# Kernel tuning notes

Hardware: AMD Instinct MI355X
Metric: run time of the kernel (lower is better)

The kernel has to match this reference:

```python
import jax, jax.numpy as jnp
import numpy as np

B, IN, OUT, E, H, K = 8192, 1024, 256, 16, 512, 3
EPS = 1e-10


def setup_inputs() -> dict:
    key = jax.random.key(0)
    ks = jax.random.split(key, 5)
    scaled = lambda k, shape, fan: jax.random.normal(k, shape, jnp.float32) / np.sqrt(fan)
    return {
        "x": jax.random.normal(ks[0], (B, IN), jnp.float32),
        # torch init is zeros for w_gate (degenerate ties); use small random for a meaningful reference
        "w_gate": jax.random.normal(ks[1], (IN, E), jnp.float32) * 0.02,
        "W1": scaled(ks[2], (E, IN, H), IN),
        "b1": jnp.zeros((E, H), jnp.float32),
        "W2": scaled(ks[3], (E, H, OUT), H),
        "b2": jnp.zeros((E, OUT), jnp.float32),
    }


def _cv_squared(v):
    # torch .var() is unbiased (ddof=1)
    return jnp.var(v, ddof=1) / (jnp.mean(v) ** 2 + EPS)


def reference(x, w_gate, W1, b1, W2, b2):
    # --- top-k gating (eval mode: clean logits, no noise) ---
    logits = x @ w_gate                                   # [B, E]
    top_vals, top_idx = jax.lax.top_k(logits, K)          # [B, K]
    top_gates = jax.nn.softmax(top_vals, axis=-1)         # softmax over selected k
    rows = jnp.arange(logits.shape[0])[:, None]
    gates = jnp.zeros_like(logits).at[rows, top_idx].set(top_gates)  # sparse gates [B, E]

    # --- load-balancing loss ---
    importance = gates.sum(0)
    load = (gates > 0).sum(0).astype(jnp.float32)         # _gates_to_load (eval path)
    loss = _cv_squared(importance) + _cv_squared(load)

    # --- experts (MLP stand-in; dense compute, sparse combine via zero gates) ---
    h = jax.nn.relu(jnp.einsum('bi,eih->beh', x, W1) + b1)  # [B, E, H]
    expert_out = jnp.einsum('beh,eho->beo', h, W2) + b2     # [B, E, OUT]

    # combine: equivalent to SparseDispatcher gather/split/scatter-add with gate weighting
    y = jnp.einsum('be,beo->bo', gates, expert_out)         # [B, OUT]
    return y, loss
```

## Files before the change

kernel.cpp:

```cpp
#include <hip/hip_runtime.h>

#define B_ 8192
#define IN_ 1024
#define OUT_ 256
#define E_ 16
#define KTOP 3
#define H_ 512
#define MAXSLOTS 26624
#define NTILES 208
#define HBLK 32
#define GBLK 512

typedef __bf16 bf16;
typedef __bf16 bf16x4 __attribute__((ext_vector_type(4)));
typedef __bf16 bf16x8 __attribute__((ext_vector_type(8)));
typedef float f32x4 __attribute__((ext_vector_type(4)));

__device__ __forceinline__ void async16(const bf16* g, bf16* l) {
    __builtin_amdgcn_global_load_lds(
        (const __attribute__((address_space(1))) void*)g,
        (__attribute__((address_space(3))) void*)l,
        16, 0, 0);
}

__global__ __launch_bounds__(256) void k_stage1(
    const float* __restrict__ x, const float* __restrict__ wg,
    const float* __restrict__ W1, const float* __restrict__ W2,
    bf16* __restrict__ xbf, int* __restrict__ top_idx, float* __restrict__ top_gate,
    int* __restrict__ partial,
    bf16* __restrict__ w1t, bf16* __restrict__ w2t,
    int* __restrict__ row_ids, bf16* __restrict__ zero_row, int* __restrict__ tile_expert) {
    __shared__ __align__(16) float smem[16448];
    __shared__ int lcnt[16];
    int bx = blockIdx.x;
    int t = threadIdx.x;
    if (bx < GBLK) {
        float4* swgT4 = (float4*)smem;
        const float4* wg4 = (const float4*)wg;
        if (t < 16) lcnt[t] = 0;
#pragma unroll
        for (int i = 0; i < 16; i++) {
            int p = (t & 3) * 4 + ((t >> 2) & 3);
            int slot = i * 16 + (t >> 4);
            swgT4[p * 257 + slot] = wg4[i * 256 + t];
        }
        __syncthreads();
        int wv = t >> 6, lane = t & 63;
#pragma unroll
        for (int pr = 0; pr < 2; ++pr) {
            int row = bx * 16 + wv * 4 + pr * 2;
            const float4* xra = (const float4*)(x + (size_t)row * IN_);
            const float4* xrb = (const float4*)(x + (size_t)(row + 1) * IN_);
            float4 xa[4], xb4[4];
#pragma unroll
            for (int q = 0; q < 4; q++) { xa[q] = xra[lane + 64 * q]; xb4[q] = xrb[lane + 64 * q]; }
#pragma unroll
            for (int q = 0; q < 4; q++) {
                bf16x4 ca, cb;
                ca[0] = (bf16)xa[q].x; ca[1] = (bf16)xa[q].y; ca[2] = (bf16)xa[q].z; ca[3] = (bf16)xa[q].w;
                cb[0] = (bf16)xb4[q].x; cb[1] = (bf16)xb4[q].y; cb[2] = (bf16)xb4[q].z; cb[3] = (bf16)xb4[q].w;
                *(bf16x4*)(xbf + (size_t)row * IN_ + (size_t)(lane + 64 * q) * 4) = ca;
                *(bf16x4*)(xbf + (size_t)(row + 1) * IN_ + (size_t)(lane + 64 * q) * 4) = cb;
            }
            float acca[16], accb[16];
#pragma unroll
            for (int e = 0; e < 16; e++) { acca[e] = 0.f; accb[e] = 0.f; }
#pragma unroll
            for (int q = 0; q < 4; q++) {
                float sa[4] = {xa[q].x, xa[q].y, xa[q].z, xa[q].w};
                float sb[4] = {xb4[q].x, xb4[q].y, xb4[q].z, xb4[q].w};
#pragma unroll
                for (int jj = 0; jj < 4; jj++) {
#pragma unroll
                    for (int e4 = 0; e4 < 4; e4++) {
                        float4 w4 = swgT4[(e4 * 4 + jj) * 257 + lane + 64 * q];
                        acca[e4 * 4 + 0] += sa[jj] * w4.x;
                        acca[e4 * 4 + 1] += sa[jj] * w4.y;
                        acca[e4 * 4 + 2] += sa[jj] * w4.z;
                        acca[e4 * 4 + 3] += sa[jj] * w4.w;
                        accb[e4 * 4 + 0] += sb[jj] * w4.x;
                        accb[e4 * 4 + 1] += sb[jj] * w4.y;
                        accb[e4 * 4 + 2] += sb[jj] * w4.z;
                        accb[e4 * 4 + 3] += sb[jj] * w4.w;
                    }
                }
            }
#pragma unroll
            for (int e = 0; e < 16; e++) {
#pragma unroll
                for (int s = 32; s > 0; s >>= 1) {
                    acca[e] += __shfl_xor(acca[e], s, 64);
                    accb[e] += __shfl_xor(accb[e], s, 64);
                }
            }
            if (lane < 2) {
                float v[16];
#pragma unroll
                for (int e = 0; e < 16; e++) v[e] = lane ? accb[e] : acca[e];
                int rsel = row + lane;
                int idx[KTOP];
                float val[KTOP];
#pragma unroll
                for (int k = 0; k < KTOP; k++) {
                    int best = 0;
                    float bv = v[0];
                    for (int e = 1; e < 16; e++) {
                        if (v[e] > bv) { bv = v[e]; best = e; }
                    }
                    idx[k] = best; val[k] = bv; v[best] = -1e30f;
                }
                float e1 = __expf(val[1] - val[0]);
                float e2 = __expf(val[2] - val[0]);
                float inv = 1.f / (1.f + e1 + e2);
                float g[KTOP] = {inv, e1 * inv, e2 * inv};
#pragma unroll
                for (int k = 0; k < KTOP; k++) {
                    top_idx[rsel * KTOP + k] = idx[k];
                    top_gate[rsel * KTOP + k] = g[k];
                    atomicAdd(&lcnt[idx[k]], 1);
                }
            }
        }
        __syncthreads();
        if (t < 16) partial[bx * 16 + t] = lcnt[t];
        return;
    }
    if (bx >= 3072) {
        if (bx < 3176) {
            row_ids[(bx - 3072) * 256 + t] = -1;
        } else {
#pragma unroll
            for (int i = 0; i < 4; i++) zero_row[t * 4 + i] = (bf16)0.f;
            if (t < NTILES) tile_expert[t] = -1;
        }
        return;
    }
    float (*tile)[65] = (float(*)[65])smem;
    const float* in; bf16* out; int Kd, Nd, e, tk, tn;
    if (bx < 2560) {
        int b1x = bx - 512;
        in = W1; out = w1t; Kd = IN_; Nd = H_;
        e = b1x >> 7; int tt = b1x & 127; tk = tt >> 3; tn = tt & 7;
    } else {
        int b2x = bx - 2560;
        in = W2; out = w2t; Kd = H_; Nd = OUT_;
        e = b2x >> 5; int tt = b2x & 31; tk = tt >> 2; tn = tt & 3;
    }
    const float* src = in + ((size_t)e * Kd + tk * 64) * Nd + (size_t)tn * 64;
    {
        int c4 = (t & 15) * 4;
#pragma unroll
        for (int p = 0; p < 4; p++) {
            int kr = p * 16 + (t >> 4);
            float4 v = *(const float4*)(src + (size_t)kr * Nd + c4);
            tile[kr][c4 + 0] = v.x;
            tile[kr][c4 + 1] = v.y;
            tile[kr][c4 + 2] = v.z;
            tile[kr][c4 + 3] = v.w;
        }
    }
    __syncthreads();
    bf16* dst = out + ((size_t)e * Nd + tn * 64) * Kd + (size_t)tk * 64;
    {
        int k8 = (t & 7) * 8;
#pragma unroll
        for (int p = 0; p < 2; p++) {
            int n = p * 32 + (t >> 3);
            bf16x8 o;
#pragma unroll
            for (int j = 0; j < 8; j++) o[j] = (bf16)tile[k8 + j][n];
            *(bf16x8*)(dst + (size_t)n * Kd + k8) = o;
        }
    }
}

__global__ __launch_bounds__(256) void k_scatterscan(
    const int* __restrict__ top_idx, const float* __restrict__ top_gate,
    const int* __restrict__ partial,
    int* __restrict__ counts, int* __restrict__ tile_expert,
    int* __restrict__ row_ids, int* __restrict__ rowslot,
    float* __restrict__ partial_imp) {
    __shared__ int segsum[32][16];
    __shared__ int tote[16];
    __shared__ int sbase[16];
    __shared__ int lcnt[16];
    __shared__ float limp[16];
    int t = threadIdx.x;
    int blk = blockIdx.x;
    int e = t & 15, sg2 = t >> 4;
#pragma unroll
    for (int h = 0; h < 2; h++) {
        int seg = sg2 + h * 16;
        int s = 0;
#pragma unroll
        for (int i = 0; i < 16; i++) s += partial[(seg * 16 + i) * 16 + e];
        segsum[seg][e] = s;
    }
    if (t < 16) { lcnt[t] = 0; limp[t] = 0.f; }
    __syncthreads();
    if (t < 16) {
        int total = 0, pre = 0;
        for (int sg = 0; sg < 32; sg++) {
            int v = segsum[sg][t];
            total += v;
            if (sg < blk) pre += v;
        }
        tote[t] = total;
        segsum[0][t] = pre;
    }
    __syncthreads();
    if (t < 16) {
        int off = 0;
        for (int ee = 0; ee < 16; ee++) {
            if (ee == t) break;
            off += (tote[ee] + 127) & ~127;
        }
        sbase[t] = off + segsum[0][t];
        if (blk == 0) {
            counts[t] = tote[t];
            int pd = (tote[t] + 127) & ~127;
            for (int tt = off >> 7; tt < (off + pd) >> 7; ++tt) tile_expert[tt] = t;
        }
    }
    __syncthreads();
#pragma unroll
    for (int j = 0; j < 3; j++) {
        int gid = blk * 768 + j * 256 + t;
        int ee = top_idx[gid];
        float g = top_gate[gid];
        int rank = atomicAdd(&lcnt[ee], 1);
        atomicAdd(&limp[ee], g);
        int slot = sbase[ee] + rank;
        row_ids[slot] = gid / KTOP;
        rowslot[gid] = slot;
    }
    __syncthreads();
    if (t < 16) partial_imp[blk * 16 + t] = limp[t];
}

#define VWAIT(N) asm volatile("s_waitcnt vmcnt(" #N ")" ::: "memory")
__global__ __launch_bounds__(512) void k_fused(
    const bf16* __restrict__ xbf, const bf16* __restrict__ w1t,
    const float* __restrict__ b1, const bf16* __restrict__ w2t,
    const float* __restrict__ b2, const int* __restrict__ row_ids,
    const int* __restrict__ tile_expert, const bf16* __restrict__ zero_row,
    bf16* __restrict__ eout) {
    int bid = blockIdx.x;
    int tile = (bid & 7) * (NTILES / 8) + (bid >> 3);
    int e = tile_expert[tile];
    if (e < 0) return;
    int slot_base = tile * 128;
    __shared__ __align__(16) bf16 smem[69632];
    bf16* hs = smem;
    bf16* pb0 = smem + 32768;
    bf16* pb1 = smem + 32768 + 12288;
    bf16* pb2 = smem + 32768 + 24576;
    int t = threadIdx.x;
    int cg = (t & 3) ^ ((t >> 3) & 3);
    int rid = row_ids[slot_base + (t >> 2)];
    const bf16* gA = ((rid >= 0) ? xbf + (size_t)rid * IN_ : zero_row) + cg * 8;
    const bf16* gB1[2];
    const bf16* gB2[2];
#pragma unroll
    for (int j = 0; j < 2; j++) {
        int m = j * 128 + (t >> 2);
        gB1[j] = w1t + ((size_t)e * H_ + m) * IN_ + cg * 8;
        gB2[j] = w2t + ((size_t)e * OUT_ + m) * H_ + cg * 8;
    }
    int w = t >> 6, lane = t & 63;
    int wm = (w & 1) * 64, wn = (w >> 1) * 64;
    int lm = lane & 15, lq = lane >> 4;
    int aidx[4], bidx[4], hrow[4], hx[4];
#pragma unroll
    for (int i = 0; i < 4; i++) {
        int ra = wm + i * 16 + lm;
        int rb = wn + i * 16 + lm;
        aidx[i] = ra * 4 + (lq ^ ((ra >> 1) & 3));
        bidx[i] = rb * 4 + (lq ^ ((rb >> 1) & 3));
        hrow[i] = ra * 32;
        hx[i] = ra & 7;
    }
    float rbias1[2][4], rbias2[4];
#pragma unroll
    for (int c2 = 0; c2 < 2; ++c2)
#pragma unroll
        for (int ni = 0; ni < 4; ++ni) rbias1[c2][ni] = b1[e * H_ + c2 * 256 + wn + ni * 16 + lm];
#pragma unroll
    for (int ni = 0; ni < 4; ++ni) rbias2[ni] = b2[e * OUT_ + wn + ni * 16 + lm];
#pragma unroll
    for (int c2 = 0; c2 < 2; ++c2)
#pragma unroll
        for (int ni = 0; ni < 4; ++ni) asm volatile("" : "+v"(rbias1[c2][ni]));
#pragma unroll
    for (int ni = 0; ni < 4; ++ni) asm volatile("" : "+v"(rbias2[ni]));

    auto stageG1 = [&](bf16* buf, int c, int k) {
        async16(gA + k * 32, buf + t * 8);
        async16(gB1[0] + (size_t)c * (256 * IN_) + k * 32, buf + 4096 + t * 8);
        async16(gB1[1] + (size_t)c * (256 * IN_) + k * 32, buf + 4096 + (512 + t) * 8);
    };
    auto stageG2 = [&](bf16* buf, int c, int s) {
        const bf16* p0 = gB2[0] + c * 256 + s * 32;
        async16(p0, buf + t * 8);
        async16(gB2[1] + c * 256 + s * 32, buf + (512 + t) * 8);
        async16(p0, buf + t * 8);
    };

    f32x4 acc2[4][4] = {};
    bf16 *bufA = pb0, *bufB = pb1, *bufC = pb2;
    stageG1(bufA, 0, 0);
    stageG1(bufB, 0, 1);
#pragma unroll
    for (int c = 0; c < 2; ++c) {
        f32x4 acc1[4][4] = {};
        for (int k = 0; k < 32; ++k) {
            VWAIT(3);
            __builtin_amdgcn_s_barrier();
            __builtin_amdgcn_sched_barrier(0);
            const bf16x8* Av = (const bf16x8*)bufA;
            const bf16x8* Bv = (const bf16x8*)(bufA + 4096);
            bf16x8 af[4], bfv[4];
#pragma unroll
            for (int i = 0; i < 4; i++) af[i] = Av[aidx[i]];
#pragma unroll
            for (int i = 0; i < 4; i++) bfv[i] = Bv[bidx[i]];
            __builtin_amdgcn_s_setprio(1);
#pragma unroll
            for (int mi = 0; mi < 4; mi++)
#pragma unroll
                for (int ni = 0; ni < 4; ni++)
                    acc1[mi][ni] = __builtin_amdgcn_mfma_f32_16x16x32_bf16(af[mi], bfv[ni], acc1[mi][ni], 0, 0, 0);
            __builtin_amdgcn_s_setprio(0);
            if (k < 30) stageG1(bufC, c, k + 2);
            else        stageG2(bufC, c, k - 30);
            bf16* tmpb = bufA; bufA = bufB; bufB = bufC; bufC = tmpb;
        }
#pragma unroll
        for (int mi = 0; mi < 4; mi++) {
#pragma unroll
            for (int ni = 0; ni < 4; ni++) {
                int col = wn + ni * 16 + lm;
                float bias = rbias1[c][ni];
#pragma unroll
                for (int r = 0; r < 4; r++) {
                    int row = wm + mi * 16 + lq * 4 + r;
                    float v = acc1[mi][ni][r] + bias;
                    v = v > 0.f ? v : 0.f;
                    hs[row * 256 + (((col >> 3) ^ (row & 7)) << 3) + (col & 7)] = (bf16)v;
                }
            }
        }
        asm volatile("s_waitcnt lgkmcnt(0)" ::: "memory");
#pragma unroll
        for (int s = 0; s < 8; ++s) {
            if (c == 1 && s == 7) { VWAIT(0); } else { VWAIT(3); }
            __builtin_amdgcn_s_barrier();
            __builtin_amdgcn_sched_barrier(0);
            const bf16x8* Hv = (const bf16x8*)hs;
            const bf16x8* B2v = (const bf16x8*)bufA;
            bf16x8 af[4], bfv[4];
#pragma unroll
            for (int i = 0; i < 4; i++) af[i] = Hv[hrow[i] + ((s * 4 + lq) ^ hx[i])];
#pragma unroll
            for (int i = 0; i < 4; i++) bfv[i] = B2v[bidx[i]];
            __builtin_amdgcn_s_setprio(1);
#pragma unroll
            for (int mi = 0; mi < 4; mi++)
#pragma unroll
                for (int ni = 0; ni < 4; ni++)
                    acc2[mi][ni] = __builtin_amdgcn_mfma_f32_16x16x32_bf16(af[mi], bfv[ni], acc2[mi][ni], 0, 0, 0);
            __builtin_amdgcn_s_setprio(0);
            if (s < 6)       stageG2(bufC, c, s + 2);
            else if (c == 0) stageG1(bufC, 1, s - 6);
            bf16* tmpb = bufA; bufA = bufB; bufB = bufC; bufC = tmpb;
        }
    }
#pragma unroll
    for (int mi = 0; mi < 4; mi++) {
#pragma unroll
        for (int ni = 0; ni < 4; ni++) {
            int colg = wn + ni * 16 + lm;
            float bias = rbias2[ni];
#pragma unroll
            for (int r = 0; r < 4; r++) {
                int rowl = wm + mi * 16 + lq * 4 + r;
                eout[(size_t)(slot_base + rowl) * OUT_ + colg] = (bf16)(acc2[mi][ni][r] + bias);
            }
        }
    }
}

__global__ __launch_bounds__(256) void k_combine(
    const bf16* __restrict__ eout, const int* __restrict__ rowslot,
    const float* __restrict__ top_gate, float* __restrict__ y,
    const float* __restrict__ partial_imp, const int* __restrict__ counts,
    float* __restrict__ loss_out) {
    int t = threadIdx.x;
    if (blockIdx.x == B_ / 4) {
        __shared__ float imp[16];
        if (t < 16) {
            float s = 0.f;
#pragma unroll
            for (int b = 0; b < HBLK; b++) s += partial_imp[b * 16 + t];
            imp[t] = s;
        }
        __syncthreads();
        if (t == 0) {
            float si = 0.f, sl = 0.f;
            for (int e = 0; e < E_; e++) { si += imp[e]; sl += (float)counts[e]; }
            float mi_ = si / (float)E_, ml_ = sl / (float)E_;
            float vi = 0.f, vl = 0.f;
            for (int e = 0; e < E_; e++) {
                float d = imp[e] - mi_; vi += d * d;
                float d2 = (float)counts[e] - ml_; vl += d2 * d2;
            }
            vi /= (float)(E_ - 1); vl /= (float)(E_ - 1);
            *loss_out = vi / (mi_ * mi_ + 1e-10f) + vl / (ml_ * ml_ + 1e-10f);
        }
        return;
    }
    int b = blockIdx.x * 4 + (t >> 6);
    int lane = t & 63;
    int s0 = rowslot[b * 3], s1 = rowslot[b * 3 + 1], s2 = rowslot[b * 3 + 2];
    float g0 = top_gate[b * 3], g1 = top_gate[b * 3 + 1], g2 = top_gate[b * 3 + 2];
    bf16x4 v0 = *(const bf16x4*)(eout + (size_t)s0 * OUT_ + lane * 4);
    bf16x4 v1 = *(const bf16x4*)(eout + (size_t)s1 * OUT_ + lane * 4);
    bf16x4 v2 = *(const bf16x4*)(eout + (size_t)s2 * OUT_ + lane * 4);
    float4 r;
    r.x = g0 * (float)v0[0] + g1 * (float)v1[0] + g2 * (float)v2[0];
    r.y = g0 * (float)v0[1] + g1 * (float)v1[1] + g2 * (float)v2[1];
    r.z = g0 * (float)v0[2] + g1 * (float)v1[2] + g2 * (float)v2[2];
    r.w = g0 * (float)v0[3] + g1 * (float)v1[3] + g2 * (float)v2[3];
    ((float4*)y)[(size_t)b * 64 + lane] = r;
}

extern "C" void kernel_launch(void* const* d_in, const int* in_sizes, int n_in,
                              void* d_out, int out_size, void* d_ws, size_t ws_size,
                              hipStream_t stream) {
    (void)in_sizes; (void)n_in; (void)out_size; (void)ws_size;
    const float* x = (const float*)d_in[0];
    const float* wgate = (const float*)d_in[1];
    const float* W1 = (const float*)d_in[2];
    const float* b1 = (const float*)d_in[3];
    const float* W2 = (const float*)d_in[4];
    const float* b2 = (const float*)d_in[5];
    float* y = (float*)d_out;

    char* p = (char*)d_ws;
    auto alloc = [&](size_t bytes) {
        char* q = p;
        p += (bytes + 255) & ~(size_t)255;
        return q;
    };
    bf16* xbf = (bf16*)alloc((size_t)B_ * IN_ * 2);
    bf16* w1t = (bf16*)alloc((size_t)E_ * H_ * IN_ * 2);
    bf16* w2t = (bf16*)alloc((size_t)E_ * OUT_ * H_ * 2);
    bf16* eout = (bf16*)alloc((size_t)MAXSLOTS * OUT_ * 2);
    int* row_ids = (int*)alloc((size_t)MAXSLOTS * 4);
    int* rowslot = (int*)alloc((size_t)B_ * KTOP * 4);
    int* top_idx = (int*)alloc((size_t)B_ * KTOP * 4);
    float* top_gate = (float*)alloc((size_t)B_ * KTOP * 4);
    int* counts = (int*)alloc(E_ * 4);
    int* partial = (int*)alloc((size_t)GBLK * E_ * 4);
    float* partial_imp = (float*)alloc(HBLK * E_ * 4);
    int* tile_expert = (int*)alloc(NTILES * 4);
    bf16* zero_row = (bf16*)alloc(IN_ * 2);

    k_stage1<<<dim3(3177), dim3(256), 0, stream>>>(
        x, wgate, W1, W2, xbf, top_idx, top_gate, partial, w1t, w2t,
        row_ids, zero_row, tile_expert);
    k_scatterscan<<<dim3(HBLK), dim3(256), 0, stream>>>(
        top_idx, top_gate, partial, counts, tile_expert, row_ids, rowslot, partial_imp);
    k_fused<<<dim3(NTILES), dim3(512), 0, stream>>>(
        xbf, w1t, b1, w2t, b2, row_ids, tile_expert, zero_row, eout);
    k_combine<<<dim3(B_ / 4 + 1), dim3(256), 0, stream>>>(
        eout, rowslot, top_gate, y, partial_imp, counts, y + (size_t)B_ * OUT_);
}
```

Baseline: 183.3 us.

## Fuse gated combine into expert GEMM epilogue via atomic adds to output

The expert kernel now multiplies each output row by its gate and atomically accumulates it straight into y, instead of writing a bf16 eout buffer that a separate combine kernel re-reads. y is zeroed by extra blocks in the first stage kernel, and the combine kernel shrinks to a one-block loss kernel. This removes the eout round trip and one large launch, but adds float atomics (three writers per token) with non-deterministic summation order and scattered per-element atomic traffic. The s_setprio hints around the MFMA loops are also dropped.

```diff
diff --git a/kernel.cpp b/kernel.cpp
--- a/kernel.cpp
+++ b/kernel.cpp
@@ -29,7 +29,8 @@
     bf16* __restrict__ xbf, int* __restrict__ top_idx, float* __restrict__ top_gate,
     int* __restrict__ partial,
     bf16* __restrict__ w1t, bf16* __restrict__ w2t,
-    int* __restrict__ row_ids, bf16* __restrict__ zero_row, int* __restrict__ tile_expert) {
+    int* __restrict__ row_ids, bf16* __restrict__ zero_row, int* __restrict__ tile_expert,
+    float* __restrict__ y) {
     __shared__ __align__(16) float smem[16448];
     __shared__ int lcnt[16];
     int bx = blockIdx.x;
@@ -128,10 +129,15 @@
     if (bx >= 3072) {
         if (bx < 3176) {
             row_ids[(bx - 3072) * 256 + t] = -1;
-        } else {
+        } else if (bx == 3176) {
 #pragma unroll
             for (int i = 0; i < 4; i++) zero_row[t * 4 + i] = (bf16)0.f;
             if (t < NTILES) tile_expert[t] = -1;
+        } else {
+            float4* y4 = (float4*)y + (size_t)(bx - 3177) * 1024;
+            float4 z = {0.f, 0.f, 0.f, 0.f};
+#pragma unroll
+            for (int i = 0; i < 4; i++) y4[i * 256 + t] = z;
         }
         return;
     }
@@ -178,7 +184,7 @@
     const int* __restrict__ top_idx, const float* __restrict__ top_gate,
     const int* __restrict__ partial,
     int* __restrict__ counts, int* __restrict__ tile_expert,
-    int* __restrict__ row_ids, int* __restrict__ rowslot,
+    int* __restrict__ row_ids, float* __restrict__ slot_gate,
     float* __restrict__ partial_imp) {
     __shared__ int segsum[32][16];
     __shared__ int tote[16];
@@ -232,7 +238,7 @@
         atomicAdd(&limp[ee], g);
         int slot = sbase[ee] + rank;
         row_ids[slot] = gid / KTOP;
-        rowslot[gid] = slot;
+        slot_gate[slot] = g;
     }
     __syncthreads();
     if (t < 16) partial_imp[blk * 16 + t] = limp[t];
@@ -243,8 +249,9 @@
     const bf16* __restrict__ xbf, const bf16* __restrict__ w1t,
     const float* __restrict__ b1, const bf16* __restrict__ w2t,
     const float* __restrict__ b2, const int* __restrict__ row_ids,
+    const float* __restrict__ slot_gate,
     const int* __restrict__ tile_expert, const bf16* __restrict__ zero_row,
-    bf16* __restrict__ eout) {
+    float* __restrict__ y) {
     int bid = blockIdx.x;
     int tile = (bid & 7) * (NTILES / 8) + (bid >> 3);
     int e = tile_expert[tile];
@@ -324,13 +331,11 @@
             for (int i = 0; i < 4; i++) af[i] = Av[aidx[i]];
 #pragma unroll
             for (int i = 0; i < 4; i++) bfv[i] = Bv[bidx[i]];
-            __builtin_amdgcn_s_setprio(1);
 #pragma unroll
             for (int mi = 0; mi < 4; mi++)
 #pragma unroll
                 for (int ni = 0; ni < 4; ni++)
                     acc1[mi][ni] = __builtin_amdgcn_mfma_f32_16x16x32_bf16(af[mi], bfv[ni], acc1[mi][ni], 0, 0, 0);
-            __builtin_amdgcn_s_setprio(0);
             if (k < 30) stageG1(bufC, c, k + 2);
             else        stageG2(bufC, c, k - 30);
             bf16* tmpb = bufA; bufA = bufB; bufB = bufC; bufC = tmpb;
@@ -363,13 +368,11 @@
             for (int i = 0; i < 4; i++) af[i] = Hv[hrow[i] + ((s * 4 + lq) ^ hx[i])];
 #pragma unroll
             for (int i = 0; i < 4; i++) bfv[i] = B2v[bidx[i]];
-            __builtin_amdgcn_s_setprio(1);
 #pragma unroll
             for (int mi = 0; mi < 4; mi++)
 #pragma unroll
                 for (int ni = 0; ni < 4; ni++)
                     acc2[mi][ni] = __builtin_amdgcn_mfma_f32_16x16x32_bf16(af[mi], bfv[ni], acc2[mi][ni], 0, 0, 0);
-            __builtin_amdgcn_s_setprio(0);
             if (s < 6)       stageG2(bufC, c, s + 2);
             else if (c == 0) stageG1(bufC, 1, s - 6);
             bf16* tmpb = bufA; bufA = bufB; bufB = bufC; bufC = tmpb;
@@ -378,60 +381,45 @@
 #pragma unroll
     for (int mi = 0; mi < 4; mi++) {
 #pragma unroll
-        for (int ni = 0; ni < 4; ni++) {
-            int colg = wn + ni * 16 + lm;
-            float bias = rbias2[ni];
-#pragma unroll
-            for (int r = 0; r < 4; r++) {
-                int rowl = wm + mi * 16 + lq * 4 + r;
-                eout[(size_t)(slot_base + rowl) * OUT_ + colg] = (bf16)(acc2[mi][ni][r] + bias);
-            }
-        }
-    }
-}
-
-__global__ __launch_bounds__(256) void k_combine(
-    const bf16* __restrict__ eout, const int* __restrict__ rowslot,
-    const float* __restrict__ top_gate, float* __restrict__ y,
+        for (int r = 0; r < 4; r++) {
+            int rowl = wm + mi * 16 + lq * 4 + r;
+            int tok = row_ids[slot_base + rowl];
+            if (tok < 0) continue;
+            float g = slot_gate[slot_base + rowl];
+            float* yr = y + (size_t)tok * OUT_;
+#pragma unroll
+            for (int ni = 0; ni < 4; ni++) {
+                int colg = wn + ni * 16 + lm;
+                atomicAdd(yr + colg, g * (acc2[mi][ni][r] + rbias2[ni]));
+            }
+        }
+    }
+}
+
+__global__ __launch_bounds__(256) void k_loss(
     const float* __restrict__ partial_imp, const int* __restrict__ counts,
     float* __restrict__ loss_out) {
     int t = threadIdx.x;
-    if (blockIdx.x == B_ / 4) {
-        __shared__ float imp[16];
-        if (t < 16) {
-            float s = 0.f;
-#pragma unroll
-            for (int b = 0; b < HBLK; b++) s += partial_imp[b * 16 + t];
-            imp[t] = s;
-        }
-        __syncthreads();
-        if (t == 0) {
-            float si = 0.f, sl = 0.f;
-            for (int e = 0; e < E_; e++) { si += imp[e]; sl += (float)counts[e]; }
-            float mi_ = si / (float)E_, ml_ = sl / (float)E_;
-            float vi = 0.f, vl = 0.f;
-            for (int e = 0; e < E_; e++) {
-                float d = imp[e] - mi_; vi += d * d;
-                float d2 = (float)counts[e] - ml_; vl += d2 * d2;
-            }
-            vi /= (float)(E_ - 1); vl /= (float)(E_ - 1);
-            *loss_out = vi / (mi_ * mi_ + 1e-10f) + vl / (ml_ * ml_ + 1e-10f);
-        }
-        return;
-    }
-    int b = blockIdx.x * 4 + (t >> 6);
-    int lane = t & 63;
-    int s0 = rowslot[b * 3], s1 = rowslot[b * 3 + 1], s2 = rowslot[b * 3 + 2];
-    float g0 = top_gate[b * 3], g1 = top_gate[b * 3 + 1], g2 = top_gate[b * 3 + 2];
-    bf16x4 v0 = *(const bf16x4*)(eout + (size_t)s0 * OUT_ + lane * 4);
-    bf16x4 v1 = *(const bf16x4*)(eout + (size_t)s1 * OUT_ + lane * 4);
-    bf16x4 v2 = *(const bf16x4*)(eout + (size_t)s2 * OUT_ + lane * 4);
-    float4 r;
-    r.x = g0 * (float)v0[0] + g1 * (float)v1[0] + g2 * (float)v2[0];
-    r.y = g0 * (float)v0[1] + g1 * (float)v1[1] + g2 * (float)v2[1];
-    r.z = g0 * (float)v0[2] + g1 * (float)v1[2] + g2 * (float)v2[2];
-    r.w = g0 * (float)v0[3] + g1 * (float)v1[3] + g2 * (float)v2[3];
-    ((float4*)y)[(size_t)b * 64 + lane] = r;
+    __shared__ float imp[16];
+    if (t < 16) {
+        float s = 0.f;
+#pragma unroll
+        for (int b = 0; b < HBLK; b++) s += partial_imp[b * 16 + t];
+        imp[t] = s;
+    }
+    __syncthreads();
+    if (t == 0) {
+        float si = 0.f, sl = 0.f;
+        for (int e = 0; e < E_; e++) { si += imp[e]; sl += (float)counts[e]; }
+        float mi_ = si / (float)E_, ml_ = sl / (float)E_;
+        float vi = 0.f, vl = 0.f;
+        for (int e = 0; e < E_; e++) {
+            float d = imp[e] - mi_; vi += d * d;
+            float d2 = (float)counts[e] - ml_; vl += d2 * d2;
+        }
+        vi /= (float)(E_ - 1); vl /= (float)(E_ - 1);
+        *loss_out = vi / (mi_ * mi_ + 1e-10f) + vl / (ml_ * ml_ + 1e-10f);
+    }
 }
 
 extern "C" void kernel_launch(void* const* d_in, const int* in_sizes, int n_in,
@@ -455,9 +443,8 @@
     bf16* xbf = (bf16*)alloc((size_t)B_ * IN_ * 2);
     bf16* w1t = (bf16*)alloc((size_t)E_ * H_ * IN_ * 2);
     bf16* w2t = (bf16*)alloc((size_t)E_ * OUT_ * H_ * 2);
-    bf16* eout = (bf16*)alloc((size_t)MAXSLOTS * OUT_ * 2);
     int* row_ids = (int*)alloc((size_t)MAXSLOTS * 4);
-    int* rowslot = (int*)alloc((size_t)B_ * KTOP * 4);
+    float* slot_gate = (float*)alloc((size_t)MAXSLOTS * 4);
     int* top_idx = (int*)alloc((size_t)B_ * KTOP * 4);
     float* top_gate = (float*)alloc((size_t)B_ * KTOP * 4);
     int* counts = (int*)alloc(E_ * 4);
@@ -466,13 +453,13 @@
     int* tile_expert = (int*)alloc(NTILES * 4);
     bf16* zero_row = (bf16*)alloc(IN_ * 2);
 
-    k_stage1<<<dim3(3177), dim3(256), 0, stream>>>(
+    k_stage1<<<dim3(3689), dim3(256), 0, stream>>>(
         x, wgate, W1, W2, xbf, top_idx, top_gate, partial, w1t, w2t,
-        row_ids, zero_row, tile_expert);
+        row_ids, zero_row, tile_expert, y);
     k_scatterscan<<<dim3(HBLK), dim3(256), 0, stream>>>(
-        top_idx, top_gate, partial, counts, tile_expert, row_ids, rowslot, partial_imp);
+        top_idx, top_gate, partial, counts, tile_expert, row_ids, slot_gate, partial_imp);
     k_fused<<<dim3(NTILES), dim3(512), 0, stream>>>(
-        xbf, w1t, b1, w2t, b2, row_ids, tile_expert, zero_row, eout);
-    k_combine<<<dim3(B_ / 4 + 1), dim3(256), 0, stream>>>(
-        eout, rowslot, top_gate, y, partial_imp, counts, y + (size_t)B_ * OUT_);
-}
+        xbf, w1t, b1, w2t, b2, row_ids, slot_gate, tile_expert, zero_row, y);
+    k_loss<<<dim3(1), dim3(256), 0, stream>>>(
+        partial_imp, counts, y + (size_t)B_ * OUT_);
+}
```

Result: slower. 193.3 us (+5.5%).
